# Optimization experiments

Hardware: AMD Instinct MI355X
Metric: run time of the kernel (lower is better)

Reference implementation:

```python
import jax, jax.numpy as jnp
import numpy as np

N, D = 512, 64          # n_objects, object_dim
HG, OG = 256, 256       # g hidden, g output
HF, OF = 256, 64        # f hidden, f output


def setup_inputs() -> dict:
    key = jax.random.key(0)
    ks = jax.random.split(key, 16)
    s = 0.05
    inp = {
        "x": jax.random.normal(ks[0], (N, D), dtype=jnp.float32),
        "q": jax.random.normal(ks[1], (D,), dtype=jnp.float32),
        # MLP g: input 3*D -> HG -> OG (ReLU after every layer, nonlinear=True)
        "g_w1": jax.random.normal(ks[2], (3 * D, HG), dtype=jnp.float32) * s,
        "g_b1": jnp.zeros((HG,), dtype=jnp.float32),
        "g_w2": jax.random.normal(ks[3], (HG, OG), dtype=jnp.float32) * s,
        "g_b2": jnp.zeros((OG,), dtype=jnp.float32),
        # query_expand: D -> HG -> OG (nonlinear=True)
        "qe_w1": jax.random.normal(ks[4], (D, HG), dtype=jnp.float32) * s,
        "qe_b1": jnp.zeros((HG,), dtype=jnp.float32),
        "qe_w2": jax.random.normal(ks[5], (HG, OG), dtype=jnp.float32) * s,
        "qe_b2": jnp.zeros((OG,), dtype=jnp.float32),
        # MLP f: OG -> HF -> OF (ReLU on hidden only, nonlinear=False)
        "f_w1": jax.random.normal(ks[6], (OG, HF), dtype=jnp.float32) * s,
        "f_b1": jnp.zeros((HF,), dtype=jnp.float32),
        "f_w2": jax.random.normal(ks[7], (HF, OF), dtype=jnp.float32) * s,
        "f_b2": jnp.zeros((OF,), dtype=jnp.float32),
    }
    return inp


def reference(x, q, g_w1, g_b1, g_w2, g_b2, qe_w1, qe_b1, qe_w2, qe_b2,
              f_w1, f_b1, f_w2, f_b2):
    n, d = x.shape
    # pair (a,b): first half x_i = x[b], second half x_j = x[a], then query q
    xi = jnp.broadcast_to(x[None, :, :], (n, n, d))   # repeats x along dim 0
    xj = jnp.broadcast_to(x[:, None, :], (n, n, d))   # repeats x along dim 1
    qb = jnp.broadcast_to(q[None, None, :], (n, n, d))
    pair_concat = jnp.concatenate([xi, xj, qb], axis=-1).reshape(n * n, 3 * d)
    # g MLP (ReLU after every layer since nonlinear=True)
    h = jax.nn.relu(pair_concat @ g_w1 + g_b1)
    relations = jax.nn.relu(h @ g_w2 + g_b2)          # [N*N, OG]
    # attentional weighting
    qh = jax.nn.relu(q @ qe_w1 + qe_b1)
    q_exp = jax.nn.relu(qh @ qe_w2 + qe_b2)           # [OG]
    c = jax.nn.softmax(relations @ q_exp, axis=0)     # [N*N]
    embedding = jnp.sum(relations * c[:, None], axis=0)  # [OG]
    # f MLP (no final nonlinearity)
    fh = jax.nn.relu(embedding @ f_w1 + f_b1)
    out = fh @ f_w2 + f_b2                            # [OF]
    return out
```

## Files before the change

kernel.cpp:

```cpp
#include <hip/hip_runtime.h>
#include <hip/hip_bf16.h>

typedef __attribute__((ext_vector_type(8))) short s16x8;
typedef __attribute__((ext_vector_type(4))) float f32x4;

#define NSLOT 128

__device__ __forceinline__ short f2bf(float f) {
    union { float f; unsigned u; } c; c.f = f;
    unsigned u = c.u;
    return (short)((u + 0x7fffu + ((u >> 16) & 1u)) >> 16);
}

__global__ __launch_bounds__(256) void rn_k1(
    const float* __restrict__ x, const float* __restrict__ q,
    const float* __restrict__ g_w1, const float* __restrict__ g_b1,
    const float* __restrict__ g_w2,
    const float* __restrict__ qe_w1, const float* __restrict__ qe_b1,
    const float* __restrict__ qe_w2, const float* __restrict__ qe_b2,
    float* __restrict__ U, float* __restrict__ V,
    float* __restrict__ c0, float* __restrict__ qexp,
    short* __restrict__ w2s, float* __restrict__ accb)
{
    __shared__ float sbuf[64];
    __shared__ float qh[256];
    const int blk = blockIdx.x, t = threadIdx.x;

    if (blk < 512) {
        if (t < 64) sbuf[t] = x[blk * 64 + t];
        __syncthreads();
        float u = 0.f, v = 0.f;
        #pragma unroll 4
        for (int k = 0; k < 64; ++k) {
            float xv = sbuf[k];
            u += xv * g_w1[k * 256 + t];
            v += xv * g_w1[(64 + k) * 256 + t];
        }
        U[blk * 256 + t] = u;
        V[blk * 256 + t] = v;
        {
            int E = blk * 256 + t;
            int e = E & 7, f = E >> 3;
            int lane = f & 63, n = (f >> 6) & 3, kk = (f >> 8) & 7, wv = (f >> 11) & 3;
            int l15 = lane & 15, g = lane >> 4;
            int col = wv * 64 + n * 16 + l15;
            int k = kk * 32 + g * 8 + e;
            w2s[E] = f2bf(g_w2[k * 256 + col]);
        }
    } else if (blk == 512) {
        if (t < 64) sbuf[t] = q[t];
        __syncthreads();
        float cc = g_b1[t], hh = qe_b1[t];
        #pragma unroll 4
        for (int k = 0; k < 64; ++k) {
            float qv = sbuf[k];
            cc += qv * g_w1[(128 + k) * 256 + t];
            hh += qv * qe_w1[k * 256 + t];
        }
        c0[t] = cc;
        qh[t] = fmaxf(hh, 0.f);
        __syncthreads();
        float qe = qe_b2[t];
        #pragma unroll 4
        for (int k = 0; k < 256; ++k) qe += qh[k] * qe_w2[k * 256 + t];
        qexp[t] = fmaxf(qe, 0.f);
    } else {
        const int total = NSLOT * 257;
        int off = (blk - 513) * 2048 + t * 8;
        #pragma unroll
        for (int i = 0; i < 8; ++i)
            if (off + i < total) accb[off + i] = 0.f;
    }
}

__global__ __launch_bounds__(256, 3) void rn_k2(
    const float* __restrict__ U, const float* __restrict__ V,
    const float* __restrict__ c0, const float* __restrict__ qexp,
    const short* __restrict__ w2s, const float* __restrict__ g_b2,
    float* __restrict__ accb)
{
    __shared__ short hT[64][264];
    __shared__ float srowT[64][4];

    const int bid = blockIdx.x;
    const int a   = bid >> 3;
    const int b0  = (bid & 7) << 6;
    const int tid = threadIdx.x;
    const int wave = tid >> 6, lane = tid & 63;
    const int l15 = lane & 15, g = lane >> 4;
    const int col0 = wave << 6;

    const short* w2w = w2s + (wave << 14);
#define BFR_LOAD(kk, n) (*(const s16x8*)&w2w[(((kk) * 4 + (n)) << 9) + (lane << 3)])

    s16x8 bfr[2][4];
    #pragma unroll
    for (int n = 0; n < 4; ++n) bfr[0][n] = BFR_LOAD(0, n);

    float qe[4], b2c[4];
    #pragma unroll
    for (int n = 0; n < 4; ++n) {
        int col = col0 + n * 16 + l15;
        qe[n]  = qexp[col];
        b2c[n] = g_b2[col];
    }

    {
        const int c4 = tid & 63;
        const int r0 = tid >> 6;
        const float4 vv  = *(const float4*)&V[a * 256 + c4 * 4];
        const float4 cc  = *(const float4*)&c0[c4 * 4];
        const float4 vcv = make_float4(vv.x + cc.x, vv.y + cc.y,
                                       vv.z + cc.z, vv.w + cc.w);
        #pragma unroll
        for (int it = 0; it < 16; ++it) {
            int row = r0 + it * 4;
            float4 uu = *(const float4*)&U[(b0 + row) * 256 + c4 * 4];
            __hip_bfloat162 p0 = __float22bfloat162_rn(
                make_float2(fmaxf(uu.x + vcv.x, 0.f), fmaxf(uu.y + vcv.y, 0.f)));
            __hip_bfloat162 p1 = __float22bfloat162_rn(
                make_float2(fmaxf(uu.z + vcv.z, 0.f), fmaxf(uu.w + vcv.w, 0.f)));
            uint2 st;
            st.x = *reinterpret_cast<unsigned*>(&p0);
            st.y = *reinterpret_cast<unsigned*>(&p1);
            *reinterpret_cast<uint2*>(&hT[row][c4 * 4]) = st;
        }
    }
    __syncthreads();

    f32x4 acc[4][4];
    #pragma unroll
    for (int m = 0; m < 4; ++m)
        #pragma unroll
        for (int n = 0; n < 4; ++n)
            acc[m][n] = (f32x4){0.f, 0.f, 0.f, 0.f};

    s16x8 afr[2][4];
    #pragma unroll
    for (int m = 0; m < 4; ++m)
        afr[0][m] = *(const s16x8*)&hT[m * 16 + l15][g * 8];

    #pragma unroll
    for (int kk = 0; kk < 8; ++kk) {
        const int cur = kk & 1, nxt = cur ^ 1;
        if (kk < 7) {
            const int koff = (kk + 1) * 32 + g * 8;
            #pragma unroll
            for (int m = 0; m < 4; ++m)
                afr[nxt][m] = *(const s16x8*)&hT[m * 16 + l15][koff];
            #pragma unroll
            for (int n = 0; n < 4; ++n)
                bfr[nxt][n] = BFR_LOAD(kk + 1, n);
        }
        #pragma unroll
        for (int n = 0; n < 4; ++n)
            #pragma unroll
            for (int m = 0; m < 4; ++m)
                acc[m][n] = __builtin_amdgcn_mfma_f32_16x16x32_bf16(
                    afr[cur][m], bfr[cur][n], acc[m][n], 0, 0, 0);
    }
#undef BFR_LOAD

    #pragma unroll
    for (int m = 0; m < 4; ++m)
        #pragma unroll
        for (int n = 0; n < 4; ++n)
            #pragma unroll
            for (int j = 0; j < 4; ++j)
                acc[m][n][j] = fmaxf(acc[m][n][j] + b2c[n], 0.f);

    #pragma unroll
    for (int m = 0; m < 4; ++m) {
        #pragma unroll
        for (int j = 0; j < 4; ++j) {
            float sp = 0.f;
            #pragma unroll
            for (int n = 0; n < 4; ++n) sp += acc[m][n][j] * qe[n];
            sp += __shfl_xor(sp, 1);
            sp += __shfl_xor(sp, 2);
            sp += __shfl_xor(sp, 4);
            sp += __shfl_xor(sp, 8);
            if (l15 == 0) srowT[m * 16 + g * 4 + j][wave] = sp;
        }
    }
    __syncthreads();

    float wrow[4][4];
    #pragma unroll
    for (int m = 0; m < 4; ++m)
        #pragma unroll
        for (int j = 0; j < 4; ++j) {
            const float4 s4 = *(const float4*)&srowT[m * 16 + g * 4 + j][0];
            wrow[m][j] = __expf(s4.x + s4.y + s4.z + s4.w);
        }

    const int slot = bid & (NSLOT - 1);
    if (wave == 0) {
        float ls = 0.f;
        #pragma unroll
        for (int m = 0; m < 4; ++m)
            #pragma unroll
            for (int j = 0; j < 4; ++j) ls += wrow[m][j];
        ls += __shfl_xor(ls, 16);
        ls += __shfl_xor(ls, 32);
        if (lane == 0) atomicAdd(&accb[slot * 257 + 256], ls);
    }

    #pragma unroll
    for (int n = 0; n < 4; ++n) {
        float wv = 0.f;
        #pragma unroll
        for (int m = 0; m < 4; ++m)
            #pragma unroll
            for (int j = 0; j < 4; ++j)
                wv += wrow[m][j] * acc[m][n][j];
        wv += __shfl_xor(wv, 16);
        wv += __shfl_xor(wv, 32);
        if (lane < 16) atomicAdd(&accb[slot * 257 + col0 + n * 16 + lane], wv);
    }
}

__global__ __launch_bounds__(256) void rn_k4(
    const float* __restrict__ accb,
    const float* __restrict__ f_w1, const float* __restrict__ f_b1,
    const float* __restrict__ f_w2, const float* __restrict__ f_b2,
    float* __restrict__ out)
{
    __shared__ float emb[256];
    __shared__ float fh[256];
    const int t = threadIdx.x;

    float v0 = 0.f, v1 = 0.f, v2 = 0.f, v3 = 0.f;
    float ls = 0.f;
    #pragma unroll
    for (int s = 0; s < NSLOT; s += 4) {
        v0 += accb[(s + 0) * 257 + t];
        v1 += accb[(s + 1) * 257 + t];
        v2 += accb[(s + 2) * 257 + t];
        v3 += accb[(s + 3) * 257 + t];
        ls += accb[s * 257 + 256] + accb[(s + 1) * 257 + 256]
            + accb[(s + 2) * 257 + 256] + accb[(s + 3) * 257 + 256];
    }
    emb[t] = (v0 + v1 + v2 + v3) / ls;
    __syncthreads();

    float h0 = f_b1[t], h1 = 0.f, h2 = 0.f, h3 = 0.f;
    #pragma unroll 8
    for (int k = 0; k < 256; k += 4) {
        h0 += emb[k + 0] * f_w1[(k + 0) * 256 + t];
        h1 += emb[k + 1] * f_w1[(k + 1) * 256 + t];
        h2 += emb[k + 2] * f_w1[(k + 2) * 256 + t];
        h3 += emb[k + 3] * f_w1[(k + 3) * 256 + t];
    }
    fh[t] = fmaxf((h0 + h1) + (h2 + h3), 0.f);
    __syncthreads();

    if (t < 64) {
        float o0 = f_b2[t], o1 = 0.f, o2 = 0.f, o3 = 0.f;
        #pragma unroll 8
        for (int k = 0; k < 256; k += 4) {
            o0 += fh[k + 0] * f_w2[(k + 0) * 64 + t];
            o1 += fh[k + 1] * f_w2[(k + 1) * 64 + t];
            o2 += fh[k + 2] * f_w2[(k + 2) * 64 + t];
            o3 += fh[k + 3] * f_w2[(k + 3) * 64 + t];
        }
        out[t] = (o0 + o1) + (o2 + o3);
    }
}

extern "C" void kernel_launch(void* const* d_in, const int* in_sizes, int n_in,
                              void* d_out, int out_size, void* d_ws, size_t ws_size,
                              hipStream_t stream) {
    const float* x     = (const float*)d_in[0];
    const float* q     = (const float*)d_in[1];
    const float* g_w1  = (const float*)d_in[2];
    const float* g_b1  = (const float*)d_in[3];
    const float* g_w2  = (const float*)d_in[4];
    const float* g_b2  = (const float*)d_in[5];
    const float* qe_w1 = (const float*)d_in[6];
    const float* qe_b1 = (const float*)d_in[7];
    const float* qe_w2 = (const float*)d_in[8];
    const float* qe_b2 = (const float*)d_in[9];
    const float* f_w1  = (const float*)d_in[10];
    const float* f_b1  = (const float*)d_in[11];
    const float* f_w2  = (const float*)d_in[12];
    const float* f_b2  = (const float*)d_in[13];

    float* wsf  = (float*)d_ws;
    float* U    = wsf;
    float* V    = wsf + 131072;
    float* c0   = wsf + 262144;
    float* qexp = wsf + 262400;
    short* w2s  = (short*)(wsf + 262656);
    float* accb = wsf + 328192;

    hipLaunchKernelGGL(rn_k1, dim3(530), dim3(256), 0, stream,
                       x, q, g_w1, g_b1, g_w2, qe_w1, qe_b1, qe_w2, qe_b2,
                       U, V, c0, qexp, w2s, accb);
    hipLaunchKernelGGL(rn_k2, dim3(4096), dim3(256), 0, stream,
                       U, V, c0, qexp, (const short*)w2s, g_b2, accb);
    hipLaunchKernelGGL(rn_k4, dim3(1), dim3(256), 0, stream,
                       accb, f_w1, f_b1, f_w2, f_b2, (float*)d_out);
}
```

Measured before the change: 74.71 us.

## Stage bf16 U tile via direct global-to-LDS loads with XOR swizzle

U is now stored in bf16, pre-swizzled by an XOR pattern, so rn_k2 can copy each 64-row U tile straight into LDS with global_load_lds. It then applies V+c0 and ReLU in place in LDS. The unpadded hT layout relies on the XOR swizzle to avoid bank conflicts, which lowers LDS use, and occupancy goes from 3 to 4 blocks. The MFMA loop drops its register double buffering and adds s_setprio around the MFMAs. Rounding U to bf16 before adding V adds a second rounding step, which slightly changes precision.

```diff
diff --git a/kernel.cpp b/kernel.cpp
--- a/kernel.cpp
+++ b/kernel.cpp
@@ -11,6 +11,19 @@
     unsigned u = c.u;
     return (short)((u + 0x7fffu + ((u >> 16) & 1u)) >> 16);
 }
+__device__ __forceinline__ float bf2f(short s) {
+    union { unsigned u; float f; } c;
+    c.u = ((unsigned)(unsigned short)s) << 16;
+    return c.f;
+}
+__device__ __forceinline__ unsigned pk2(float lo, float hi) {
+    __hip_bfloat162 p = __float22bfloat162_rn(make_float2(lo, hi));
+    return *reinterpret_cast<unsigned*>(&p);
+}
+
+#define GLD16(gp, lp) __builtin_amdgcn_global_load_lds( \
+    (const __attribute__((address_space(1))) unsigned int*)(gp), \
+    (__attribute__((address_space(3))) unsigned int*)(lp), 16, 0, 0)
 
 __global__ __launch_bounds__(256) void rn_k1(
     const float* __restrict__ x, const float* __restrict__ q,
@@ -18,7 +31,7 @@
     const float* __restrict__ g_w2,
     const float* __restrict__ qe_w1, const float* __restrict__ qe_b1,
     const float* __restrict__ qe_w2, const float* __restrict__ qe_b2,
-    float* __restrict__ U, float* __restrict__ V,
+    short* __restrict__ u8, float* __restrict__ V,
     float* __restrict__ c0, float* __restrict__ qexp,
     short* __restrict__ w2s, float* __restrict__ accb)
 {
@@ -36,7 +49,7 @@
             u += xv * g_w1[k * 256 + t];
             v += xv * g_w1[(64 + k) * 256 + t];
         }
-        U[blk * 256 + t] = u;
+        u8[blk * 256 + (t ^ ((blk & 7) << 3))] = f2bf(u);
         V[blk * 256 + t] = v;
         {
             int E = blk * 256 + t;
@@ -73,13 +86,13 @@
     }
 }
 
-__global__ __launch_bounds__(256, 3) void rn_k2(
-    const float* __restrict__ U, const float* __restrict__ V,
-    const float* __restrict__ c0, const float* __restrict__ qexp,
+__global__ __launch_bounds__(256, 4) void rn_k2(
+    const float* __restrict__ V, const float* __restrict__ c0,
+    const float* __restrict__ qexp, const short* __restrict__ u8,
     const short* __restrict__ w2s, const float* __restrict__ g_b2,
     float* __restrict__ accb)
 {
-    __shared__ short hT[64][264];
+    __shared__ short hT[64 * 256];
     __shared__ float srowT[64][4];
 
     const int bid = blockIdx.x;
@@ -90,12 +103,28 @@
     const int l15 = lane & 15, g = lane >> 4;
     const int col0 = wave << 6;
 
-    const short* w2w = w2s + (wave << 14);
-#define BFR_LOAD(kk, n) (*(const s16x8*)&w2w[(((kk) * 4 + (n)) << 9) + (lane << 3)])
-
-    s16x8 bfr[2][4];
-    #pragma unroll
-    for (int n = 0; n < 4; ++n) bfr[0][n] = BFR_LOAD(0, n);
+    {
+        const short* src = u8 + b0 * 256;
+        #pragma unroll
+        for (int i = 0; i < 8; ++i) {
+            const int j = wave * 8 + i;
+            GLD16(src + j * 512 + lane * 8, hT + j * 512);
+        }
+    }
+
+    const int rowb = tid >> 5;
+    const int colb = ((tid & 31) * 8) ^ (rowb << 3);
+    float vc8[8];
+    {
+        const float4 vA = *(const float4*)&V[a * 256 + colb];
+        const float4 vB = *(const float4*)&V[a * 256 + colb + 4];
+        const float4 cA = *(const float4*)&c0[colb];
+        const float4 cB = *(const float4*)&c0[colb + 4];
+        vc8[0] = vA.x + cA.x; vc8[1] = vA.y + cA.y;
+        vc8[2] = vA.z + cA.z; vc8[3] = vA.w + cA.w;
+        vc8[4] = vB.x + cB.x; vc8[5] = vB.y + cB.y;
+        vc8[6] = vB.z + cB.z; vc8[7] = vB.w + cB.w;
+    }
 
     float qe[4], b2c[4];
     #pragma unroll
@@ -105,28 +134,31 @@
         b2c[n] = g_b2[col];
     }
 
-    {
-        const int c4 = tid & 63;
-        const int r0 = tid >> 6;
-        const float4 vv  = *(const float4*)&V[a * 256 + c4 * 4];
-        const float4 cc  = *(const float4*)&c0[c4 * 4];
-        const float4 vcv = make_float4(vv.x + cc.x, vv.y + cc.y,
-                                       vv.z + cc.z, vv.w + cc.w);
-        #pragma unroll
-        for (int it = 0; it < 16; ++it) {
-            int row = r0 + it * 4;
-            float4 uu = *(const float4*)&U[(b0 + row) * 256 + c4 * 4];
-            __hip_bfloat162 p0 = __float22bfloat162_rn(
-                make_float2(fmaxf(uu.x + vcv.x, 0.f), fmaxf(uu.y + vcv.y, 0.f)));
-            __hip_bfloat162 p1 = __float22bfloat162_rn(
-                make_float2(fmaxf(uu.z + vcv.z, 0.f), fmaxf(uu.w + vcv.w, 0.f)));
-            uint2 st;
-            st.x = *reinterpret_cast<unsigned*>(&p0);
-            st.y = *reinterpret_cast<unsigned*>(&p1);
-            *reinterpret_cast<uint2*>(&hT[row][c4 * 4]) = st;
-        }
-    }
-    __syncthreads();
+    __syncthreads();
+
+    #pragma unroll
+    for (int it = 0; it < 8; ++it) {
+        const int si = tid * 8 + it * 2048;
+        s16x8 raw = *(const s16x8*)&hT[si];
+        float h0 = fmaxf(bf2f(raw[0]) + vc8[0], 0.f);
+        float h1 = fmaxf(bf2f(raw[1]) + vc8[1], 0.f);
+        float h2 = fmaxf(bf2f(raw[2]) + vc8[2], 0.f);
+        float h3 = fmaxf(bf2f(raw[3]) + vc8[3], 0.f);
+        float h4 = fmaxf(bf2f(raw[4]) + vc8[4], 0.f);
+        float h5 = fmaxf(bf2f(raw[5]) + vc8[5], 0.f);
+        float h6 = fmaxf(bf2f(raw[6]) + vc8[6], 0.f);
+        float h7 = fmaxf(bf2f(raw[7]) + vc8[7], 0.f);
+        uint4 ov;
+        ov.x = pk2(h0, h1); ov.y = pk2(h2, h3);
+        ov.z = pk2(h4, h5); ov.w = pk2(h6, h7);
+        *reinterpret_cast<uint4*>(&hT[si]) = ov;
+    }
+    __syncthreads();
+
+    const short* w2w = w2s + (wave << 14);
+#define BFR_LOAD(kk, n) (*(const s16x8*)&w2w[(((kk) * 4 + (n)) << 9) + (lane << 3)])
+    const int axor  = (l15 & 7) << 3;
+    const int arow0 = l15 * 256;
 
     f32x4 acc[4][4];
     #pragma unroll
@@ -135,29 +167,24 @@
         for (int n = 0; n < 4; ++n)
             acc[m][n] = (f32x4){0.f, 0.f, 0.f, 0.f};
 
-    s16x8 afr[2][4];
-    #pragma unroll
-    for (int m = 0; m < 4; ++m)
-        afr[0][m] = *(const s16x8*)&hT[m * 16 + l15][g * 8];
-
     #pragma unroll
     for (int kk = 0; kk < 8; ++kk) {
-        const int cur = kk & 1, nxt = cur ^ 1;
-        if (kk < 7) {
-            const int koff = (kk + 1) * 32 + g * 8;
-            #pragma unroll
-            for (int m = 0; m < 4; ++m)
-                afr[nxt][m] = *(const s16x8*)&hT[m * 16 + l15][koff];
+        const int koff = kk * 32 + g * 8;
+        s16x8 bfr[4];
+        #pragma unroll
+        for (int n = 0; n < 4; ++n) bfr[n] = BFR_LOAD(kk, n);
+        s16x8 afr[4];
+        #pragma unroll
+        for (int m = 0; m < 4; ++m)
+            afr[m] = *(const s16x8*)&hT[arow0 + m * 4096 + (koff ^ axor)];
+        __builtin_amdgcn_s_setprio(1);
+        #pragma unroll
+        for (int m = 0; m < 4; ++m)
             #pragma unroll
             for (int n = 0; n < 4; ++n)
-                bfr[nxt][n] = BFR_LOAD(kk + 1, n);
-        }
-        #pragma unroll
-        for (int n = 0; n < 4; ++n)
-            #pragma unroll
-            for (int m = 0; m < 4; ++m)
                 acc[m][n] = __builtin_amdgcn_mfma_f32_16x16x32_bf16(
-                    afr[cur][m], bfr[cur][n], acc[m][n], 0, 0, 0);
+                    afr[m], bfr[n], acc[m][n], 0, 0, 0);
+        __builtin_amdgcn_s_setprio(0);
     }
 #undef BFR_LOAD
 
@@ -287,18 +314,18 @@
     const float* f_b2  = (const float*)d_in[13];
 
     float* wsf  = (float*)d_ws;
-    float* U    = wsf;
-    float* V    = wsf + 131072;
-    float* c0   = wsf + 262144;
-    float* qexp = wsf + 262400;
-    short* w2s  = (short*)(wsf + 262656);
-    float* accb = wsf + 328192;
+    short* u8   = (short*)wsf;
+    float* V    = wsf + 65536;
+    float* c0   = wsf + 196608;
+    float* qexp = wsf + 196864;
+    short* w2s  = (short*)(wsf + 197120);
+    float* accb = wsf + 229888;
 
     hipLaunchKernelGGL(rn_k1, dim3(530), dim3(256), 0, stream,
                        x, q, g_w1, g_b1, g_w2, qe_w1, qe_b1, qe_w2, qe_b2,
-                       U, V, c0, qexp, w2s, accb);
+                       u8, V, c0, qexp, w2s, accb);
     hipLaunchKernelGGL(rn_k2, dim3(4096), dim3(256), 0, stream,
-                       U, V, c0, qexp, (const short*)w2s, g_b2, accb);
+                       V, c0, qexp, (const short*)u8, (const short*)w2s, g_b2, accb);
     hipLaunchKernelGGL(rn_k4, dim3(1), dim3(256), 0, stream,
                        accb, f_w1, f_b1, f_w2, f_b2, (float*)d_out);
 }
```

Result: faster. 72.10 us (-3.5%).
